# Kernel tuning notes

Measured on AMD Instinct MI355X. Metric: run time of the kernel, lower is better.

The kernel has to match this reference:

```python
import jax, jax.numpy as jnp
import numpy as np

N = 1048576   # total points
B = 4096      # samples
C = 96        # backbone_out_channels
K = 4         # num refinement heads
OUT = 3
EPS = 1e-5    # torch LayerNorm default


def _ln(x, g, b):
    m = jnp.mean(x, axis=-1, keepdims=True)
    v = jnp.mean((x - m) ** 2, axis=-1, keepdims=True)
    return (x - m) * jax.lax.rsqrt(v + EPS) * g + b


def setup_inputs() -> dict:
    key = jax.random.key(0)
    ks = jax.random.split(key, 16)
    s = 0.05
    f32 = jnp.float32
    inp = {
        'feat': jax.random.normal(ks[0], (N, C), f32),
        'segment_ids': jnp.sort(jax.random.randint(ks[1], (N,), 0, B, dtype=jnp.int32)),
        'class_ids': jax.random.randint(ks[2], (B,), 0, K, dtype=jnp.int32),
        # coarse head: Linear(96,256) LN ReLU  Linear(256,128) LN ReLU  Linear(128,3)
        'cW1': jax.random.normal(ks[3], (C, 256), f32) * s, 'cb1': jnp.zeros(256, f32),
        'cg1': jnp.ones(256, f32), 'cbe1': jnp.zeros(256, f32),
        'cW2': jax.random.normal(ks[4], (256, 128), f32) * s, 'cb2': jnp.zeros(128, f32),
        'cg2': jnp.ones(128, f32), 'cbe2': jnp.zeros(128, f32),
        'cW3': jax.random.normal(ks[5], (128, OUT), f32) * s, 'cb3': jnp.zeros(OUT, f32),
        # 4 refinement heads, stacked on leading axis k
        'rW1': jax.random.normal(ks[6], (K, C, 128), f32) * s, 'rb1': jnp.zeros((K, 128), f32),
        'rg1': jnp.ones((K, 128), f32), 'rbe1': jnp.zeros((K, 128), f32),
        'rW2': jax.random.normal(ks[7], (K, 128, 64), f32) * s, 'rb2': jnp.zeros((K, 64), f32),
        'rg2': jnp.ones((K, 64), f32), 'rbe2': jnp.zeros((K, 64), f32),
        'rW3': jax.random.normal(ks[8], (K, 64, OUT), f32) * s, 'rb3': jnp.zeros((K, OUT), f32),
    }
    return inp


def reference(feat, segment_ids, class_ids,
              cW1, cb1, cg1, cbe1, cW2, cb2, cg2, cbe2, cW3, cb3,
              rW1, rb1, rg1, rbe1, rW2, rb2, rg2, rbe2, rW3, rb3):
    # segment_csr(mean): mean-pool per-sample point features -> [B, C]
    summed = jax.ops.segment_sum(feat, segment_ids, num_segments=B, indices_are_sorted=True)
    counts = jax.ops.segment_sum(jnp.ones((N,), feat.dtype), segment_ids,
                                 num_segments=B, indices_are_sorted=True)
    pooled = summed / jnp.maximum(counts, 1.0)[:, None]

    # coarse head (dropout is identity in eval)
    h = jax.nn.relu(_ln(pooled @ cW1 + cb1, cg1, cbe1))
    h = jax.nn.relu(_ln(h @ cW2 + cb2, cg2, cbe2))
    coarse = h @ cW3 + cb3  # [B, 3]

    # per-class refinement: run all 4 tiny heads batched, then route by class id
    r = jnp.einsum('bc,kcd->kbd', pooled, rW1) + rb1[:, None, :]
    r = jax.nn.relu(_ln(r, rg1[:, None, :], rbe1[:, None, :]))
    r = jnp.einsum('kbd,kde->kbe', r, rW2) + rb2[:, None, :]
    r = jax.nn.relu(_ln(r, rg2[:, None, :], rbe2[:, None, :]))
    r = jnp.einsum('kbe,keo->kbo', r, rW3) + rb3[:, None, :]  # [K, B, 3]
    offsets = r[class_ids, jnp.arange(B)]  # route each sample to its class head

    return coarse + offsets  # bracket_point_pred [B, 3]
```

## Files before the change

kernel.cpp:

```cpp
#include <hip/hip_runtime.h>

#define N_PTS 1048576
#define B_SEG 4096
#define C_IN  96
#define LN_EPS 1e-5f

__device__ __forceinline__ int lower_bound_i(const int* __restrict__ a, int n, int v){
  int lo = 0, hi = n;
  while(lo < hi){
    int m = (lo + hi) >> 1;
    if(a[m] < v) lo = m + 1; else hi = m;
  }
  return lo;
}

__device__ __forceinline__ float f4e(const float4& v, int j){
  return j==0 ? v.x : j==1 ? v.y : j==2 ? v.z : v.w;
}

__global__ __launch_bounds__(192) void pool_kernel(
    const float* __restrict__ feat, const int* __restrict__ seg,
    float* __restrict__ pooled)
{
  const int b   = blockIdx.x;
  const int tid = threadIdx.x;
  const int lo  = lower_bound_i(seg, N_PTS, b);
  const int hi  = lower_bound_i(seg, N_PTS, b + 1);
  const int g = tid % 24;
  const int r = tid / 24;
  const float4* __restrict__ f4 = (const float4*)feat;
  float ax = 0.f, ay = 0.f, az = 0.f, aw = 0.f;
  for(int row = lo + r; row < hi; row += 8){
    float4 v = f4[(size_t)row * 24 + g];
    ax += v.x; ay += v.y; az += v.z; aw += v.w;
  }
  __shared__ float4 part[192];
  part[tid] = make_float4(ax, ay, az, aw);
  __syncthreads();
  if(tid < 24){
    float sx=0.f, sy=0.f, sz=0.f, sw=0.f;
    #pragma unroll
    for(int rr=0; rr<8; rr++){
      float4 v = part[rr*24 + tid];
      sx += v.x; sy += v.y; sz += v.z; sw += v.w;
    }
    int cnt = hi - lo; if(cnt < 1) cnt = 1;
    float inv = 1.f / (float)cnt;
    ((float4*)pooled)[b*24 + tid] = make_float4(sx*inv, sy*inv, sz*inv, sw*inv);
  }
}

__global__ __launch_bounds__(256) void mlp_kernel(
    const float* __restrict__ pooled, const int* __restrict__ class_ids,
    const float* __restrict__ cW1, const float* __restrict__ cb1,
    const float* __restrict__ cg1, const float* __restrict__ cbe1,
    const float* __restrict__ cW2, const float* __restrict__ cb2,
    const float* __restrict__ cg2, const float* __restrict__ cbe2,
    const float* __restrict__ cW3, const float* __restrict__ cb3,
    const float* __restrict__ rW1, const float* __restrict__ rb1,
    const float* __restrict__ rg1, const float* __restrict__ rbe1,
    const float* __restrict__ rW2, const float* __restrict__ rb2,
    const float* __restrict__ rg2, const float* __restrict__ rbe2,
    const float* __restrict__ rW3, const float* __restrict__ rb3,
    float* __restrict__ out)
{
  const int tid = threadIdx.x;
  const int blk = blockIdx.x;
  const int b0  = blk * 8;
  const int lane = tid & 63;
  const int wv   = tid >> 6;

  __shared__ float p   [8*96];
  __shared__ float h1  [8*256];
  __shared__ float h2  [8*132];
  __shared__ float r1b [8*128];
  __shared__ float r2b [8*68];
  __shared__ float couts[24];
  __shared__ int   kcls[8];
  __shared__ float redbuf[4][32];
  __shared__ float stats[32];

  for(int i = tid; i < 8*96; i += 256) p[i] = pooled[b0*96 + i];
  if(tid < 8) kcls[tid] = class_ids[b0 + tid];
  __syncthreads();

  {
    const int o = tid;
    float acc[8];
    float bias = cb1[o];
    #pragma unroll
    for(int s=0;s<8;s++) acc[s] = bias;
    for(int c0=0;c0<96;c0+=4){
      float4 pv[8];
      #pragma unroll
      for(int s=0;s<8;s++) pv[s] = *(const float4*)&p[s*96 + c0];
      #pragma unroll
      for(int j=0;j<4;j++){
        float w = cW1[(c0+j)*256 + o];
        #pragma unroll
        for(int s=0;s<8;s++) acc[s] = fmaf(f4e(pv[s], j), w, acc[s]);
      }
    }
    float sum[8], sq[8];
    #pragma unroll
    for(int s=0;s<8;s++){ sum[s]=acc[s]; sq[s]=acc[s]*acc[s]; }
    #pragma unroll
    for(int m=32;m>=1;m>>=1){
      #pragma unroll
      for(int s=0;s<8;s++){
        sum[s] += __shfl_xor(sum[s], m, 64);
        sq[s]  += __shfl_xor(sq[s],  m, 64);
      }
    }
    if(lane == 0){
      #pragma unroll
      for(int s=0;s<8;s++){ redbuf[wv][s]=sum[s]; redbuf[wv][8+s]=sq[s]; }
    }
    __syncthreads();
    if(tid < 16) stats[tid] = redbuf[0][tid]+redbuf[1][tid]+redbuf[2][tid]+redbuf[3][tid];
    __syncthreads();
    float gg = cg1[o], be = cbe1[o];
    #pragma unroll
    for(int s=0;s<8;s++){
      float mean = stats[s]   * (1.f/256.f);
      float var  = stats[8+s] * (1.f/256.f) - mean*mean;
      float rstd = rsqrtf(var + LN_EPS);
      float v = (acc[s]-mean)*rstd*gg + be;
      h1[s*256 + o] = v > 0.f ? v : 0.f;
    }
    __syncthreads();
  }

  {
    const int o = tid & 127;
    const int g = tid >> 7;
    float acc[4];
    float bias = cb2[o];
    #pragma unroll
    for(int s=0;s<4;s++) acc[s] = bias;
    for(int c0=0;c0<256;c0+=4){
      float4 hv[4];
      #pragma unroll
      for(int s=0;s<4;s++) hv[s] = *(const float4*)&h1[(g*4+s)*256 + c0];
      #pragma unroll
      for(int j=0;j<4;j++){
        float w = cW2[(c0+j)*128 + o];
        #pragma unroll
        for(int s=0;s<4;s++) acc[s] = fmaf(f4e(hv[s], j), w, acc[s]);
      }
    }
    float sum[4], sq[4];
    #pragma unroll
    for(int s=0;s<4;s++){ sum[s]=acc[s]; sq[s]=acc[s]*acc[s]; }
    #pragma unroll
    for(int m=32;m>=1;m>>=1){
      #pragma unroll
      for(int s=0;s<4;s++){
        sum[s] += __shfl_xor(sum[s], m, 64);
        sq[s]  += __shfl_xor(sq[s],  m, 64);
      }
    }
    if(lane == 0){
      #pragma unroll
      for(int s=0;s<4;s++){ redbuf[wv][s]=sum[s]; redbuf[wv][4+s]=sq[s]; }
    }
    __syncthreads();
    if(tid < 16){ int gq = tid>>3, i = tid&7; stats[tid] = redbuf[2*gq][i] + redbuf[2*gq+1][i]; }
    __syncthreads();
    float gg = cg2[o], be = cbe2[o];
    #pragma unroll
    for(int s=0;s<4;s++){
      float mean = stats[g*8+s]   * (1.f/128.f);
      float var  = stats[g*8+4+s] * (1.f/128.f) - mean*mean;
      float rstd = rsqrtf(var + LN_EPS);
      float v = (acc[s]-mean)*rstd*gg + be;
      h2[(g*4+s)*132 + o] = v > 0.f ? v : 0.f;
    }
    __syncthreads();
  }

  if(tid < 24){
    int s = tid/3, j = tid - 3*(tid/3);
    float a = cb3[j];
    for(int c=0;c<128;c++) a = fmaf(h2[s*132 + c], cW3[c*3 + j], a);
    couts[tid] = a;
  }

  {
    const int o = tid & 127;
    const int g = tid >> 7;
    int ks[4]; const float* wp[4]; float acc[4];
    #pragma unroll
    for(int s=0;s<4;s++){
      ks[s]  = kcls[g*4+s];
      wp[s]  = rW1 + ks[s]*(96*128) + o;
      acc[s] = rb1[ks[s]*128 + o];
    }
    for(int c0=0;c0<96;c0+=4){
      float4 pv[4];
      #pragma unroll
      for(int s=0;s<4;s++) pv[s] = *(const float4*)&p[(g*4+s)*96 + c0];
      #pragma unroll
      for(int j=0;j<4;j++){
        #pragma unroll
        for(int s=0;s<4;s++){
          float w = wp[s][(c0+j)*128];
          acc[s] = fmaf(f4e(pv[s], j), w, acc[s]);
        }
      }
    }
    float sum[4], sq[4];
    #pragma unroll
    for(int s=0;s<4;s++){ sum[s]=acc[s]; sq[s]=acc[s]*acc[s]; }
    #pragma unroll
    for(int m=32;m>=1;m>>=1){
      #pragma unroll
      for(int s=0;s<4;s++){
        sum[s] += __shfl_xor(sum[s], m, 64);
        sq[s]  += __shfl_xor(sq[s],  m, 64);
      }
    }
    if(lane == 0){
      #pragma unroll
      for(int s=0;s<4;s++){ redbuf[wv][s]=sum[s]; redbuf[wv][4+s]=sq[s]; }
    }
    __syncthreads();
    if(tid < 16){ int gq = tid>>3, i = tid&7; stats[tid] = redbuf[2*gq][i] + redbuf[2*gq+1][i]; }
    __syncthreads();
    #pragma unroll
    for(int s=0;s<4;s++){
      float mean = stats[g*8+s]   * (1.f/128.f);
      float var  = stats[g*8+4+s] * (1.f/128.f) - mean*mean;
      float rstd = rsqrtf(var + LN_EPS);
      float v = (acc[s]-mean)*rstd*rg1[ks[s]*128+o] + rbe1[ks[s]*128+o];
      r1b[(g*4+s)*128 + o] = v > 0.f ? v : 0.f;
    }
    __syncthreads();
  }

  {
    const int o = tid & 63;
    const int g = tid >> 6;
    int ks[2]; const float* wp[2]; float acc[2];
    #pragma unroll
    for(int s=0;s<2;s++){
      ks[s]  = kcls[g*2+s];
      wp[s]  = rW2 + ks[s]*(128*64) + o;
      acc[s] = rb2[ks[s]*64 + o];
    }
    for(int c0=0;c0<128;c0+=4){
      float4 rv[2];
      #pragma unroll
      for(int s=0;s<2;s++) rv[s] = *(const float4*)&r1b[(g*2+s)*128 + c0];
      #pragma unroll
      for(int j=0;j<4;j++){
        #pragma unroll
        for(int s=0;s<2;s++){
          float w = wp[s][(c0+j)*64];
          acc[s] = fmaf(f4e(rv[s], j), w, acc[s]);
        }
      }
    }
    float sum[2], sq[2];
    #pragma unroll
    for(int s=0;s<2;s++){ sum[s]=acc[s]; sq[s]=acc[s]*acc[s]; }
    #pragma unroll
    for(int m=32;m>=1;m>>=1){
      #pragma unroll
      for(int s=0;s<2;s++){
        sum[s] += __shfl_xor(sum[s], m, 64);
        sq[s]  += __shfl_xor(sq[s],  m, 64);
      }
    }
    #pragma unroll
    for(int s=0;s<2;s++){
      float mean = sum[s] * (1.f/64.f);
      float var  = sq[s]  * (1.f/64.f) - mean*mean;
      float rstd = rsqrtf(var + LN_EPS);
      float v = (acc[s]-mean)*rstd*rg2[ks[s]*64+o] + rbe2[ks[s]*64+o];
      r2b[(g*2+s)*68 + o] = v > 0.f ? v : 0.f;
    }
    __syncthreads();
  }

  if(tid < 24){
    int s = tid/3, j = tid - 3*(tid/3);
    int k = kcls[s];
    float a = rb3[k*3 + j];
    const float* w = rW3 + k*192 + j;
    for(int c=0;c<64;c++) a = fmaf(r2b[s*68 + c], w[c*3], a);
    out[(b0+s)*3 + j] = a + couts[tid];
  }
}

extern "C" void kernel_launch(void* const* d_in, const int* in_sizes, int n_in,
                              void* d_out, int out_size, void* d_ws, size_t ws_size,
                              hipStream_t stream)
{
  const float* feat = (const float*)d_in[0];
  const int*   seg  = (const int*)d_in[1];
  const int*   cls  = (const int*)d_in[2];
  const float* cW1  = (const float*)d_in[3];
  const float* cb1  = (const float*)d_in[4];
  const float* cg1  = (const float*)d_in[5];
  const float* cbe1 = (const float*)d_in[6];
  const float* cW2  = (const float*)d_in[7];
  const float* cb2  = (const float*)d_in[8];
  const float* cg2  = (const float*)d_in[9];
  const float* cbe2 = (const float*)d_in[10];
  const float* cW3  = (const float*)d_in[11];
  const float* cb3  = (const float*)d_in[12];
  const float* rW1  = (const float*)d_in[13];
  const float* rb1  = (const float*)d_in[14];
  const float* rg1  = (const float*)d_in[15];
  const float* rbe1 = (const float*)d_in[16];
  const float* rW2  = (const float*)d_in[17];
  const float* rb2  = (const float*)d_in[18];
  const float* rg2  = (const float*)d_in[19];
  const float* rbe2 = (const float*)d_in[20];
  const float* rW3  = (const float*)d_in[21];
  const float* rb3  = (const float*)d_in[22];
  float* out    = (float*)d_out;
  float* pooled = (float*)d_ws;

  pool_kernel<<<B_SEG, 192, 0, stream>>>(feat, seg, pooled);
  mlp_kernel<<<B_SEG/8, 256, 0, stream>>>(pooled, cls,
      cW1, cb1, cg1, cbe1, cW2, cb2, cg2, cbe2, cW3, cb3,
      rW1, rb1, rg1, rbe1, rW2, rb2, rg2, rbe2, rW3, rb3, out);
}
```

Baseline: 611.2 us.

## Fuse segment mean-pooling into the MLP kernel, four samples per block

Merges the pooling kernel and the MLP kernel into one launch. Each 256-thread block now finds five segment boundaries, reduces four segments with 240 threads into shared memory, and then runs both heads on those four pooled rows. This removes the pooled round trip through global memory and one kernel launch. In exchange, the 1024 blocks each stream four segments with only 240 loading threads, so memory parallelism per sample drops and the MLP weight reads are shared across fewer samples.

```diff
diff --git a/kernel.cpp b/kernel.cpp
--- a/kernel.cpp
+++ b/kernel.cpp
@@ -2,7 +2,6 @@
 
 #define N_PTS 1048576
 #define B_SEG 4096
-#define C_IN  96
 #define LN_EPS 1e-5f
 
 __device__ __forceinline__ int lower_bound_i(const int* __restrict__ a, int n, int v){
@@ -18,40 +17,9 @@
   return j==0 ? v.x : j==1 ? v.y : j==2 ? v.z : v.w;
 }
 
-__global__ __launch_bounds__(192) void pool_kernel(
+__global__ __launch_bounds__(256, 4) void fused_kernel(
     const float* __restrict__ feat, const int* __restrict__ seg,
-    float* __restrict__ pooled)
-{
-  const int b   = blockIdx.x;
-  const int tid = threadIdx.x;
-  const int lo  = lower_bound_i(seg, N_PTS, b);
-  const int hi  = lower_bound_i(seg, N_PTS, b + 1);
-  const int g = tid % 24;
-  const int r = tid / 24;
-  const float4* __restrict__ f4 = (const float4*)feat;
-  float ax = 0.f, ay = 0.f, az = 0.f, aw = 0.f;
-  for(int row = lo + r; row < hi; row += 8){
-    float4 v = f4[(size_t)row * 24 + g];
-    ax += v.x; ay += v.y; az += v.z; aw += v.w;
-  }
-  __shared__ float4 part[192];
-  part[tid] = make_float4(ax, ay, az, aw);
-  __syncthreads();
-  if(tid < 24){
-    float sx=0.f, sy=0.f, sz=0.f, sw=0.f;
-    #pragma unroll
-    for(int rr=0; rr<8; rr++){
-      float4 v = part[rr*24 + tid];
-      sx += v.x; sy += v.y; sz += v.z; sw += v.w;
-    }
-    int cnt = hi - lo; if(cnt < 1) cnt = 1;
-    float inv = 1.f / (float)cnt;
-    ((float4*)pooled)[b*24 + tid] = make_float4(sx*inv, sy*inv, sz*inv, sw*inv);
-  }
-}
-
-__global__ __launch_bounds__(256) void mlp_kernel(
-    const float* __restrict__ pooled, const int* __restrict__ class_ids,
+    const int* __restrict__ class_ids,
     const float* __restrict__ cW1, const float* __restrict__ cb1,
     const float* __restrict__ cg1, const float* __restrict__ cbe1,
     const float* __restrict__ cW2, const float* __restrict__ cb2,
@@ -64,64 +32,109 @@
     const float* __restrict__ rW3, const float* __restrict__ rb3,
     float* __restrict__ out)
 {
-  const int tid = threadIdx.x;
-  const int blk = blockIdx.x;
-  const int b0  = blk * 8;
+  const int tid  = threadIdx.x;
+  const int b0   = blockIdx.x * 4;
   const int lane = tid & 63;
   const int wv   = tid >> 6;
 
-  __shared__ float p   [8*96];
-  __shared__ float h1  [8*256];
-  __shared__ float h2  [8*132];
-  __shared__ float r1b [8*128];
-  __shared__ float r2b [8*68];
-  __shared__ float couts[24];
-  __shared__ int   kcls[8];
+  __shared__ int    bnd[5];
+  __shared__ int    kcls[4];
+  __shared__ float4 part[960];
+  __shared__ __align__(16) float p  [4*96];
+  __shared__ __align__(16) float h1 [4*256];
+  __shared__ float h2 [4*132];
+  __shared__ __align__(16) float r1b[4*128];
+  __shared__ float r2b[4*68];
+  __shared__ float couts[12];
   __shared__ float redbuf[4][32];
   __shared__ float stats[32];
 
-  for(int i = tid; i < 8*96; i += 256) p[i] = pooled[b0*96 + i];
-  if(tid < 8) kcls[tid] = class_ids[b0 + tid];
+  if(tid < 5)              bnd[tid]      = lower_bound_i(seg, N_PTS, b0 + tid);
+  if(tid >= 8 && tid < 12) kcls[tid - 8] = class_ids[b0 + tid - 8];
   __syncthreads();
 
   {
+    const int g = tid % 24;
+    const int r = tid / 24;
+    const int e0 = bnd[0], e1 = bnd[1], e2 = bnd[2], e3 = bnd[3], e4 = bnd[4];
+    const float4* __restrict__ f4 = (const float4*)feat;
+    if(r < 10){
+      float4 a0 = make_float4(0.f,0.f,0.f,0.f), a1 = a0, a2 = a0, a3 = a0;
+      for(int row = e0 + r; row < e1; row += 10){
+        float4 v = f4[(size_t)row*24 + g];
+        a0.x += v.x; a0.y += v.y; a0.z += v.z; a0.w += v.w;
+      }
+      for(int row = e1 + r; row < e2; row += 10){
+        float4 v = f4[(size_t)row*24 + g];
+        a1.x += v.x; a1.y += v.y; a1.z += v.z; a1.w += v.w;
+      }
+      for(int row = e2 + r; row < e3; row += 10){
+        float4 v = f4[(size_t)row*24 + g];
+        a2.x += v.x; a2.y += v.y; a2.z += v.z; a2.w += v.w;
+      }
+      for(int row = e3 + r; row < e4; row += 10){
+        float4 v = f4[(size_t)row*24 + g];
+        a3.x += v.x; a3.y += v.y; a3.z += v.z; a3.w += v.w;
+      }
+      part[      tid] = a0;
+      part[240 + tid] = a1;
+      part[480 + tid] = a2;
+      part[720 + tid] = a3;
+    }
+    __syncthreads();
+    if(tid < 96){
+      const int s = tid / 24, gc = tid % 24;
+      float sx=0.f, sy=0.f, sz=0.f, sw=0.f;
+      #pragma unroll
+      for(int rr=0; rr<10; rr++){
+        float4 v = part[s*240 + rr*24 + gc];
+        sx += v.x; sy += v.y; sz += v.z; sw += v.w;
+      }
+      int cnt = bnd[s+1] - bnd[s]; if(cnt < 1) cnt = 1;
+      float inv = 1.f / (float)cnt;
+      ((float4*)p)[s*24 + gc] = make_float4(sx*inv, sy*inv, sz*inv, sw*inv);
+    }
+    __syncthreads();
+  }
+
+  {
     const int o = tid;
-    float acc[8];
+    float acc[4];
     float bias = cb1[o];
     #pragma unroll
-    for(int s=0;s<8;s++) acc[s] = bias;
+    for(int s=0;s<4;s++) acc[s] = bias;
     for(int c0=0;c0<96;c0+=4){
-      float4 pv[8];
-      #pragma unroll
-      for(int s=0;s<8;s++) pv[s] = *(const float4*)&p[s*96 + c0];
+      float4 pv[4];
+      #pragma unroll
+      for(int s=0;s<4;s++) pv[s] = *(const float4*)&p[s*96 + c0];
       #pragma unroll
       for(int j=0;j<4;j++){
         float w = cW1[(c0+j)*256 + o];
         #pragma unroll
-        for(int s=0;s<8;s++) acc[s] = fmaf(f4e(pv[s], j), w, acc[s]);
-      }
-    }
-    float sum[8], sq[8];
-    #pragma unroll
-    for(int s=0;s<8;s++){ sum[s]=acc[s]; sq[s]=acc[s]*acc[s]; }
+        for(int s=0;s<4;s++) acc[s] = fmaf(f4e(pv[s], j), w, acc[s]);
+      }
+    }
+    float sum[4], sq[4];
+    #pragma unroll
+    for(int s=0;s<4;s++){ sum[s]=acc[s]; sq[s]=acc[s]*acc[s]; }
     #pragma unroll
     for(int m=32;m>=1;m>>=1){
       #pragma unroll
-      for(int s=0;s<8;s++){
+      for(int s=0;s<4;s++){
         sum[s] += __shfl_xor(sum[s], m, 64);
         sq[s]  += __shfl_xor(sq[s],  m, 64);
       }
     }
     if(lane == 0){
       #pragma unroll
-      for(int s=0;s<8;s++){ redbuf[wv][s]=sum[s]; redbuf[wv][8+s]=sq[s]; }
+      for(int s=0;s<4;s++){ redbuf[wv][s]=sum[s]; redbuf[wv][8+s]=sq[s]; }
     }
     __syncthreads();
     if(tid < 16) stats[tid] = redbuf[0][tid]+redbuf[1][tid]+redbuf[2][tid]+redbuf[3][tid];
     __syncthreads();
     float gg = cg1[o], be = cbe1[o];
     #pragma unroll
-    for(int s=0;s<8;s++){
+    for(int s=0;s<4;s++){
       float mean = stats[s]   * (1.f/256.f);
       float var  = stats[8+s] * (1.f/256.f) - mean*mean;
       float rstd = rsqrtf(var + LN_EPS);
@@ -134,52 +147,52 @@
   {
     const int o = tid & 127;
     const int g = tid >> 7;
-    float acc[4];
+    float acc[2];
     float bias = cb2[o];
     #pragma unroll
-    for(int s=0;s<4;s++) acc[s] = bias;
+    for(int s=0;s<2;s++) acc[s] = bias;
     for(int c0=0;c0<256;c0+=4){
-      float4 hv[4];
-      #pragma unroll
-      for(int s=0;s<4;s++) hv[s] = *(const float4*)&h1[(g*4+s)*256 + c0];
+      float4 hv[2];
+      #pragma unroll
+      for(int s=0;s<2;s++) hv[s] = *(const float4*)&h1[(g*2+s)*256 + c0];
       #pragma unroll
       for(int j=0;j<4;j++){
         float w = cW2[(c0+j)*128 + o];
         #pragma unroll
-        for(int s=0;s<4;s++) acc[s] = fmaf(f4e(hv[s], j), w, acc[s]);
-      }
-    }
-    float sum[4], sq[4];
-    #pragma unroll
-    for(int s=0;s<4;s++){ sum[s]=acc[s]; sq[s]=acc[s]*acc[s]; }
+        for(int s=0;s<2;s++) acc[s] = fmaf(f4e(hv[s], j), w, acc[s]);
+      }
+    }
+    float sum[2], sq[2];
+    #pragma unroll
+    for(int s=0;s<2;s++){ sum[s]=acc[s]; sq[s]=acc[s]*acc[s]; }
     #pragma unroll
     for(int m=32;m>=1;m>>=1){
       #pragma unroll
-      for(int s=0;s<4;s++){
+      for(int s=0;s<2;s++){
         sum[s] += __shfl_xor(sum[s], m, 64);
         sq[s]  += __shfl_xor(sq[s],  m, 64);
       }
     }
     if(lane == 0){
       #pragma unroll
-      for(int s=0;s<4;s++){ redbuf[wv][s]=sum[s]; redbuf[wv][4+s]=sq[s]; }
-    }
-    __syncthreads();
-    if(tid < 16){ int gq = tid>>3, i = tid&7; stats[tid] = redbuf[2*gq][i] + redbuf[2*gq+1][i]; }
+      for(int s=0;s<2;s++){ redbuf[wv][s]=sum[s]; redbuf[wv][2+s]=sq[s]; }
+    }
+    __syncthreads();
+    if(tid < 8){ int gq = tid>>2, i = tid&3; stats[tid] = redbuf[2*gq][i] + redbuf[2*gq+1][i]; }
     __syncthreads();
     float gg = cg2[o], be = cbe2[o];
     #pragma unroll
-    for(int s=0;s<4;s++){
-      float mean = stats[g*8+s]   * (1.f/128.f);
-      float var  = stats[g*8+4+s] * (1.f/128.f) - mean*mean;
+    for(int s=0;s<2;s++){
+      float mean = stats[g*4+s]   * (1.f/128.f);
+      float var  = stats[g*4+2+s] * (1.f/128.f) - mean*mean;
       float rstd = rsqrtf(var + LN_EPS);
       float v = (acc[s]-mean)*rstd*gg + be;
-      h2[(g*4+s)*132 + o] = v > 0.f ? v : 0.f;
-    }
-    __syncthreads();
-  }
-
-  if(tid < 24){
+      h2[(g*2+s)*132 + o] = v > 0.f ? v : 0.f;
+    }
+    __syncthreads();
+  }
+
+  if(tid < 12){
     int s = tid/3, j = tid - 3*(tid/3);
     float a = cb3[j];
     for(int c=0;c<128;c++) a = fmaf(h2[s*132 + c], cW3[c*3 + j], a);
@@ -189,78 +202,26 @@
   {
     const int o = tid & 127;
     const int g = tid >> 7;
-    int ks[4]; const float* wp[4]; float acc[4];
-    #pragma unroll
-    for(int s=0;s<4;s++){
-      ks[s]  = kcls[g*4+s];
+    int ks[2]; const float* wp[2]; float acc[2];
+    #pragma unroll
+    for(int s=0;s<2;s++){
+      ks[s]  = kcls[g*2+s];
       wp[s]  = rW1 + ks[s]*(96*128) + o;
       acc[s] = rb1[ks[s]*128 + o];
     }
     for(int c0=0;c0<96;c0+=4){
-      float4 pv[4];
-      #pragma unroll
-      for(int s=0;s<4;s++) pv[s] = *(const float4*)&p[(g*4+s)*96 + c0];
+      float4 pv[2];
+      #pragma unroll
+      for(int s=0;s<2;s++) pv[s] = *(const float4*)&p[(g*2+s)*96 + c0];
       #pragma unroll
       for(int j=0;j<4;j++){
         #pragma unroll
-        for(int s=0;s<4;s++){
+        for(int s=0;s<2;s++){
           float w = wp[s][(c0+j)*128];
           acc[s] = fmaf(f4e(pv[s], j), w, acc[s]);
         }
       }
     }
-    float sum[4], sq[4];
-    #pragma unroll
-    for(int s=0;s<4;s++){ sum[s]=acc[s]; sq[s]=acc[s]*acc[s]; }
-    #pragma unroll
-    for(int m=32;m>=1;m>>=1){
-      #pragma unroll
-      for(int s=0;s<4;s++){
-        sum[s] += __shfl_xor(sum[s], m, 64);
-        sq[s]  += __shfl_xor(sq[s],  m, 64);
-      }
-    }
-    if(lane == 0){
-      #pragma unroll
-      for(int s=0;s<4;s++){ redbuf[wv][s]=sum[s]; redbuf[wv][4+s]=sq[s]; }
-    }
-    __syncthreads();
-    if(tid < 16){ int gq = tid>>3, i = tid&7; stats[tid] = redbuf[2*gq][i] + redbuf[2*gq+1][i]; }
-    __syncthreads();
-    #pragma unroll
-    for(int s=0;s<4;s++){
-      float mean = stats[g*8+s]   * (1.f/128.f);
-      float var  = stats[g*8+4+s] * (1.f/128.f) - mean*mean;
-      float rstd = rsqrtf(var + LN_EPS);
-      float v = (acc[s]-mean)*rstd*rg1[ks[s]*128+o] + rbe1[ks[s]*128+o];
-      r1b[(g*4+s)*128 + o] = v > 0.f ? v : 0.f;
-    }
-    __syncthreads();
-  }
-
-  {
-    const int o = tid & 63;
-    const int g = tid >> 6;
-    int ks[2]; const float* wp[2]; float acc[2];
-    #pragma unroll
-    for(int s=0;s<2;s++){
-      ks[s]  = kcls[g*2+s];
-      wp[s]  = rW2 + ks[s]*(128*64) + o;
-      acc[s] = rb2[ks[s]*64 + o];
-    }
-    for(int c0=0;c0<128;c0+=4){
-      float4 rv[2];
-      #pragma unroll
-      for(int s=0;s<2;s++) rv[s] = *(const float4*)&r1b[(g*2+s)*128 + c0];
-      #pragma unroll
-      for(int j=0;j<4;j++){
-        #pragma unroll
-        for(int s=0;s<2;s++){
-          float w = wp[s][(c0+j)*64];
-          acc[s] = fmaf(f4e(rv[s], j), w, acc[s]);
-        }
-      }
-    }
     float sum[2], sq[2];
     #pragma unroll
     for(int s=0;s<2;s++){ sum[s]=acc[s]; sq[s]=acc[s]*acc[s]; }
@@ -272,18 +233,50 @@
         sq[s]  += __shfl_xor(sq[s],  m, 64);
       }
     }
+    if(lane == 0){
+      #pragma unroll
+      for(int s=0;s<2;s++){ redbuf[wv][s]=sum[s]; redbuf[wv][2+s]=sq[s]; }
+    }
+    __syncthreads();
+    if(tid < 8){ int gq = tid>>2, i = tid&3; stats[tid] = redbuf[2*gq][i] + redbuf[2*gq+1][i]; }
+    __syncthreads();
     #pragma unroll
     for(int s=0;s<2;s++){
-      float mean = sum[s] * (1.f/64.f);
-      float var  = sq[s]  * (1.f/64.f) - mean*mean;
+      float mean = stats[g*4+s]   * (1.f/128.f);
+      float var  = stats[g*4+2+s] * (1.f/128.f) - mean*mean;
       float rstd = rsqrtf(var + LN_EPS);
-      float v = (acc[s]-mean)*rstd*rg2[ks[s]*64+o] + rbe2[ks[s]*64+o];
-      r2b[(g*2+s)*68 + o] = v > 0.f ? v : 0.f;
-    }
-    __syncthreads();
-  }
-
-  if(tid < 24){
+      float v = (acc[s]-mean)*rstd*rg1[ks[s]*128+o] + rbe1[ks[s]*128+o];
+      r1b[(g*2+s)*128 + o] = v > 0.f ? v : 0.f;
+    }
+    __syncthreads();
+  }
+
+  {
+    const int o = tid & 63;
+    const int g = wv;
+    const int k = kcls[g];
+    float acc = rb2[k*64 + o];
+    const float* wp = rW2 + k*(128*64) + o;
+    for(int c0=0;c0<128;c0+=4){
+      float4 rv = *(const float4*)&r1b[g*128 + c0];
+      #pragma unroll
+      for(int j=0;j<4;j++) acc = fmaf(f4e(rv, j), wp[(c0+j)*64], acc);
+    }
+    float sum = acc, sq = acc*acc;
+    #pragma unroll
+    for(int m=32;m>=1;m>>=1){
+      sum += __shfl_xor(sum, m, 64);
+      sq  += __shfl_xor(sq,  m, 64);
+    }
+    float mean = sum * (1.f/64.f);
+    float var  = sq  * (1.f/64.f) - mean*mean;
+    float rstd = rsqrtf(var + LN_EPS);
+    float v = (acc-mean)*rstd*rg2[k*64+o] + rbe2[k*64+o];
+    r2b[g*68 + o] = v > 0.f ? v : 0.f;
+    __syncthreads();
+  }
+
+  if(tid < 12){
     int s = tid/3, j = tid - 3*(tid/3);
     int k = kcls[s];
     float a = rb3[k*3 + j];
@@ -320,11 +313,10 @@
   const float* rbe2 = (const float*)d_in[20];
   const float* rW3  = (const float*)d_in[21];
   const float* rb3  = (const float*)d_in[22];
-  float* out    = (float*)d_out;
-  float* pooled = (float*)d_ws;
-
-  pool_kernel<<<B_SEG, 192, 0, stream>>>(feat, seg, pooled);
-  mlp_kernel<<<B_SEG/8, 256, 0, stream>>>(pooled, cls,
+  float* out = (float*)d_out;
+  (void)d_ws; (void)ws_size;
+
+  fused_kernel<<<B_SEG/4, 256, 0, stream>>>(feat, seg, cls,
       cW1, cb1, cg1, cbe1, cW2, cb2, cg2, cbe2, cW3, cb3,
       rW1, rb1, rg1, rbe1, rW2, rb2, rg2, rbe2, rW3, rb3, out);
 }
```

New measurement: 601.4 us. About the same (-1.6%).
